# Kernel tuning notes

Hardware: AMD Instinct MI355X
Metric: run time of the kernel (lower is better)

The kernel has to match this reference:

```python
import jax, jax.numpy as jnp
import numpy as np

EMB = 300; H = 150; DEC = 300
VU = 50000; VQ = 30000; VS = 5000
N_COLS = 64; COL_LEN = 6; N_TURNS = 6; IN_LEN = 128; GEN_LEN = 64
MAX_KEEP = 5


def _lstm_cell(x, h, c, Wih, Whh, b):
    z = x @ Wih.T + h @ Whh.T + b
    i, f, g, o = jnp.split(z, 4)
    c = jax.nn.sigmoid(f) * c + jax.nn.sigmoid(i) * jnp.tanh(g)
    h = jax.nn.sigmoid(o) * jnp.tanh(c)
    return h, c


def _run_lstm(xs, Wih, Whh, b):
    hsz = Whh.shape[-1]
    z = jnp.zeros((hsz,), xs.dtype)
    def step(carry, x):
        h, c = _lstm_cell(x, carry[0], carry[1], Wih, Whh, b)
        return (h, c), h
    (h, c), ys = jax.lax.scan(step, (z, z), xs)
    return ys, h, c


def _bilstm(xs, Wih, Whh, b):
    # Wih: [2, 4H, in], Whh: [2, 4H, H], b: [2, 4H]
    yf, hf, cf = _run_lstm(xs, Wih[0], Whh[0], b[0])
    yb, hb, cb = _run_lstm(xs[::-1], Wih[1], Whh[1], b[1])
    return jnp.concatenate([yf, yb[::-1]], -1), jnp.concatenate([hf, hb], -1), jnp.concatenate([cf, cb], -1)


def _attention(q, keys, Wq, Wk, v):
    # Bahdanau: v^T tanh(Wq q + Wk k); context = softmax-weighted sum of keys
    s = jnp.tanh(q @ Wq + keys @ Wk) @ v
    return jax.nn.softmax(s) @ keys


def _forward(utter_emb, query_emb, schema_tok_emb, enc_Wih, enc_Whh, enc_b,
             attn_Wq, attn_Wk, attn_v, dec_Wih0, dec_Whh0, dec_b0,
             dec_Wih1, dec_Whh1, dec_b1, transform_W, sql_W, sql_b, col_W,
             schema_tokens, input_seqs, output_gt):
    attn = lambda k_i, q, keys: _attention(q, keys, attn_Wq[k_i], attn_Wk[k_i], attn_v[k_i])
    # --- schema column encoding: BiLSTM over each column's name tokens ---
    col_tok = schema_tok_emb[schema_tokens]                       # [C, L, EMB]
    _, h, _ = jax.vmap(lambda xs: _bilstm(xs, enc_Wih[0], enc_Whh[0], enc_b[0]))(col_tok)
    schema_embs = h                                               # [C, EMB]
    prev_in, prev_h, prev_c, prev_out = [], [], [], []
    all_dists = []
    bos_emb = query_emb[0]
    for i in range(N_TURNS):
        idx = input_seqs[i]
        # mixed vocab / schema-pointer embedding lookup
        x = jnp.where((idx < VU)[:, None],
                      utter_emb[jnp.clip(idx, 0, VU - 1)],
                      schema_embs[jnp.clip(idx - VU, 0, N_COLS - 1)])
        x, _, _ = _bilstm(x, enc_Wih[1], enc_Whh[1], enc_b[1])    # utter_encoder
        # TextSchemaEncoder (approx): second BiLSTM + schema cross-attention update
        x, fh, fc = _bilstm(x, enc_Wih[2], enc_Whh[2], enc_b[2])
        schema_embs = schema_embs + jax.nn.softmax(schema_embs @ x.T, -1) @ x
        h0, c0 = fh, fc
        if i > 0:
            hist_h = jnp.stack(prev_h); hist_c = jnp.stack(prev_c)
            h0n = h0 + attn(0, h0, hist_h)
            c0 = h0n + attn(0, c0, hist_c)  # replicates original's h-based c init
            h0 = h0n
        prev_in = (prev_in + [x])[:MAX_KEEP]
        prev_h = (prev_h + [fh])[:MAX_KEEP]
        prev_c = (prev_c + [fc])[:MAX_KEEP]
        keys_in = jnp.concatenate(prev_in, 0)
        keys_out = jnp.concatenate(prev_out, 0) if i > 0 else None
        se = schema_embs

        def embed_out(t):
            return jnp.where(t < VQ,
                             query_emb[jnp.clip(t, 0, VQ - 1)],
                             se[jnp.clip(t - VQ, 0, N_COLS - 1)])

        def dec_step(carry, t):
            h1p, c1p, h2p, c2p, dh = carry
            out_emb = embed_out(t)  # teacher forcing
            ctx_s = attn(1, dh, se)
            ctx_i = attn(2, dh, keys_in)
            ctx_o = attn(3, dh, keys_out) if keys_out is not None else jnp.zeros_like(ctx_i)
            ctx = jnp.concatenate([ctx_s, ctx_i, ctx_o])
            xin = jnp.concatenate([out_emb, ctx])                 # [4*EMB]
            h1, c1 = _lstm_cell(xin, h1p, c1p, dec_Wih0, dec_Whh0, dec_b0)
            h2, c2 = _lstm_cell(h1, h2p, c2p, dec_Wih1, dec_Whh1, dec_b1)
            out = jnp.tanh(jnp.concatenate([h2, ctx]) @ transform_W.T)
            score = jnp.concatenate([out @ sql_W.T + sql_b, (out @ col_W.T) @ se.T])
            dist = jax.nn.log_softmax(score)
            am_emb = embed_out(jnp.argmax(dist))
            return (h1, c1, h2, c2, h2), (dist, am_emb)

        init = (h0, c0, h0, c0, h0)
        _, (dists, am_embs) = jax.lax.scan(dec_step, init, output_gt[i, :GEN_LEN - 1])
        prev_out = (prev_out + [jnp.concatenate([bos_emb[None], am_embs], 0)])[:MAX_KEEP]
        all_dists.append(dists)
    return jnp.stack(all_dists, 0)  # [N_TURNS, GEN_LEN-1, VQ+N_COLS]


def setup_inputs() -> dict:
    key = jax.random.key(0)
    ks = jax.random.split(key, 24)
    s = 0.05
    f = lambda k, shape: jax.random.normal(k, shape, jnp.float32) * s
    return {
        "utter_emb": f(ks[0], (VU, EMB)),
        "query_emb": f(ks[1], (VQ, EMB)),
        "schema_tok_emb": f(ks[2], (VS, EMB)),
        "enc_Wih": f(ks[3], (3, 2, 4 * H, EMB)),   # [schema, utter, text-schema] x [fwd, bwd]
        "enc_Whh": f(ks[4], (3, 2, 4 * H, H)),
        "enc_b": f(ks[5], (3, 2, 4 * H)),
        "attn_Wq": f(ks[6], (4, EMB, EMB)),        # [turn, schema, in_tok, out_tok]
        "attn_Wk": f(ks[7], (4, EMB, EMB)),
        "attn_v": f(ks[8], (4, EMB)),
        "dec_Wih0": f(ks[9], (4 * DEC, 4 * EMB)),
        "dec_Whh0": f(ks[10], (4 * DEC, DEC)),
        "dec_b0": f(ks[11], (4 * DEC,)),
        "dec_Wih1": f(ks[12], (4 * DEC, DEC)),
        "dec_Whh1": f(ks[13], (4 * DEC, DEC)),
        "dec_b1": f(ks[14], (4 * DEC,)),
        "transform_W": f(ks[15], (EMB, 4 * EMB)),
        "sql_W": f(ks[16], (VQ, EMB)),
        "sql_b": f(ks[17], (VQ,)),
        "col_W": f(ks[18], (EMB, EMB)),
        "schema_tokens": jax.random.randint(ks[19], (N_COLS, COL_LEN), 0, VS),
        "input_seqs": jax.random.randint(ks[20], (N_TURNS, IN_LEN), 0, VU + N_COLS),
        "output_gt": jax.random.randint(ks[21], (N_TURNS, GEN_LEN), 0, VQ + N_COLS),
    }


def reference(utter_emb, query_emb, schema_tok_emb, enc_Wih, enc_Whh, enc_b,
              attn_Wq, attn_Wk, attn_v, dec_Wih0, dec_Whh0, dec_b0,
              dec_Wih1, dec_Whh1, dec_b1, transform_W, sql_W, sql_b, col_W,
              schema_tokens, input_seqs, output_gt):
    return _forward(utter_emb, query_emb, schema_tok_emb, enc_Wih, enc_Whh, enc_b,
                    attn_Wq, attn_Wk, attn_v, dec_Wih0, dec_Whh0, dec_b0,
                    dec_Wih1, dec_Whh1, dec_b1, transform_W, sql_W, sql_b, col_W,
                    schema_tokens, input_seqs, output_gt)
```

## Files before the change

### kernel.cpp

```cpp
#include <hip/hip_runtime.h>

#define EMB 300
#define VU 50000
#define VQ 30000
#define NCOLS 64
#define COLLEN 6
#define NTURNS 6
#define INLEN 128
#define TSTEPS 63
#define VOUT 30064
#define MAXK 5
#define NWD 60
#define FPAD 32
#define SENTU 0x7FC00001u
#define NGRP 8
#define GQW (TSTEPS*960)
#define GSC (TSTEPS*1024)
#define GH  (TSTEPS*320)

__device__ __forceinline__ float sigf(float x){ return 1.0f/(1.0f+__expf(-x)); }
__device__ __forceinline__ float tanhf_(float x){ return 1.0f - 2.0f/(1.0f+__expf(2.0f*x)); }
__device__ __forceinline__ float wsum(float v){
#pragma unroll
  for (int o=32;o;o>>=1) v += __shfl_xor(v,o);
  return v;
}
__device__ __forceinline__ float wmax(float v){
#pragma unroll
  for (int o=32;o;o>>=1) v = fmaxf(v,__shfl_xor(v,o));
  return v;
}

__device__ __forceinline__ void gstore(float* p, float v){
  __hip_atomic_store((int*)p, __float_as_int(v), __ATOMIC_RELAXED, __HIP_MEMORY_SCOPE_AGENT);
}
__device__ __forceinline__ float gload(const float* p){
  return __int_as_float(__hip_atomic_load((const int*)p, __ATOMIC_RELAXED, __HIP_MEMORY_SCOPE_AGENT));
}
__device__ __forceinline__ void gpub(float* p, float v){
  (void)__hip_atomic_exchange((int*)p, __float_as_int(v), __ATOMIC_RELAXED, __HIP_MEMORY_SCOPE_AGENT);
}

__device__ __forceinline__ void garrive(int* flags, int w, int P){
  asm volatile("s_waitcnt vmcnt(0)" ::: "memory");
  __syncthreads();
  if (threadIdx.x == 0)
    __hip_atomic_store(flags + w*FPAD, P, __ATOMIC_RELAXED, __HIP_MEMORY_SCOPE_AGENT);
}
__device__ __forceinline__ void gwait(const int* flags, int P){
  if (threadIdx.x < 64) {
    int v;
    do {
      v = (threadIdx.x < NWD) ? __hip_atomic_load(flags + threadIdx.x*FPAD, __ATOMIC_RELAXED, __HIP_MEMORY_SCOPE_AGENT) : P;
    } while (__any(v < P));
  }
  __syncthreads();
}

template<int MAXV>
__device__ __forceinline__ void pollfetch(const float* __restrict__ src, float* dstLDS,
                                          int n, int modstride, int tid)
{
  float v[MAXV]; bool val[MAXV]; int idx[MAXV];
#pragma unroll
  for (int k = 0; k < MAXV; ++k) {
    idx[k] = tid + 256*k;
    bool ib = idx[k] < n;
    if (modstride) {
      int m = idx[k];
      while (m >= modstride) m -= modstride;
      ib = ib && (m < 300);
    }
    val[k] = ib;
  }
  for (;;) {
    bool ok = true;
#pragma unroll
    for (int k = 0; k < MAXV; ++k)
      if (val[k]) { v[k] = gload(src + idx[k]); ok = ok && (__float_as_uint(v[k]) != SENTU); }
    if (__all(ok)) break;
    __builtin_amdgcn_s_sleep(1);
  }
#pragma unroll
  for (int k = 0; k < MAXV; ++k) if (val[k]) dstLDS[idx[k]] = v[k];
  __syncthreads();
}

__global__ void k_init(int* flags){
  for (int i = threadIdx.x; i < NWD*FPAD; i += 256) flags[i] = 0;
}

__global__ void k_transposeB(const float* __restrict__ in, float* __restrict__ out,
                             int R, int C, size_t mstride)
{
  __shared__ float tile[32][33];
  const float* inp = in + (size_t)blockIdx.z*mstride;
  float* outp = out + (size_t)blockIdx.z*mstride;
  const int rb = blockIdx.y*32, cb = blockIdx.x*32;
  const int tx = threadIdx.x & 31, ty = threadIdx.x >> 5;
  for (int k = 0; k < 32; k += 8) {
    int r = rb + ty + k, c = cb + tx;
    if (r < R && c < C) tile[ty+k][tx] = inp[(size_t)r*C + c];
  }
  __syncthreads();
  for (int k = 0; k < 32; k += 8) {
    int c = cb + ty + k, r = rb + tx;
    if (c < C && r < R) outp[(size_t)c*R + r] = tile[tx][ty+k];
  }
}

__global__ void k_schema(const float* __restrict__ temb, const int* __restrict__ stok,
                         const float* __restrict__ Wih, const float* __restrict__ Whh,
                         const float* __restrict__ bb, float* __restrict__ SE0)
{
  const int col = blockIdx.x >> 1, dir = blockIdx.x & 1, tid = threadIdx.x;
  __shared__ float hl[150], cl[150], zl[600], xs[304];
  if (tid < 150) { hl[tid]=0.f; cl[tid]=0.f; }
  __syncthreads();
  const float* Wi = Wih + (size_t)dir*600*300;
  const float* Wh = Whh + (size_t)dir*600*150;
  const float* bd = bb + dir*600;
  for (int s = 0; s < COLLEN; ++s) {
    const int pos = dir ? (COLLEN-1-s) : s;
    const int tok = stok[col*COLLEN + pos];
    const float* x = temb + (size_t)tok*300;
    for (int c = tid; c < 300; c += 256) xs[c] = x[c];
    __syncthreads();
    for (int g = tid; g < 600; g += 256) {
      float a = bd[g];
      const float* wi = Wi + (size_t)g*300;
      for (int c = 0; c < 300; ++c) a += xs[c]*wi[c];
      const float* wh = Wh + (size_t)g*150;
      for (int j = 0; j < 150; ++j) a += hl[j]*wh[j];
      zl[g] = a;
    }
    __syncthreads();
    if (tid < 150) {
      float ii=zl[tid], ff=zl[150+tid], gg=zl[300+tid], oo=zl[450+tid];
      float cn = sigf(ff)*cl[tid] + sigf(ii)*tanhf_(gg);
      cl[tid]=cn; hl[tid]=sigf(oo)*tanhf_(cn);
    }
    __syncthreads();
  }
  if (tid < 150) SE0[(size_t)col*300 + dir*150 + tid] = hl[tid];
}

__global__ void k_gemm_xe(const float* __restrict__ src, const float* __restrict__ SEi,
                          const int* __restrict__ iseq, int mode,
                          const float* __restrict__ WihT, const float* __restrict__ bL,
                          float* __restrict__ Xg)
{
  __shared__ float xs[16][304];
  const int tid = threadIdx.x;
  const int p0 = blockIdx.y*16;
  for (int i = tid; i < 16*300; i += 256) {
    int t = i / 300, c = i - t*300;
    const float* xr;
    if (mode) xr = src + (size_t)(p0+t)*300;
    else {
      int tok = iseq[p0+t];
      xr = (tok < VU) ? src + (size_t)tok*300 : SEi + (size_t)(tok - VU)*300;
    }
    xs[t][c] = xr[c];
  }
  __syncthreads();
  const int g = blockIdx.x*256 + tid;
  if (g >= 1200) return;
  const float b = bL[g];
  float acc[16];
#pragma unroll
  for (int t = 0; t < 16; ++t) acc[t] = b;
  for (int c = 0; c < 300; ++c) {
    float wv = WihT[(size_t)c*1200 + g];
#pragma unroll
    for (int t = 0; t < 16; ++t) acc[t] += wv * xs[t][c];
  }
#pragma unroll
  for (int t = 0; t < 16; ++t) Xg[(size_t)(p0+t)*1200 + g] = acc[t];
}

__global__ __launch_bounds__(640) void k_rec(
    const float* __restrict__ Xg, const float* __restrict__ WhhTL,
    float* __restrict__ ys, float* __restrict__ fh, float* __restrict__ fc)
{
  const int dir = blockIdx.x, tid = threadIdx.x;
  __shared__ __align__(16) float hl[2][152];
  const int g = (tid & 3)*150 + (tid >> 2);
  const bool act = (tid < 600);
  float w[150];
  const float* wt = WhhTL + (size_t)dir*150*600;
  if (act) {
#pragma unroll
    for (int j = 0; j < 150; ++j) w[j] = wt[(size_t)j*600 + g];
  }
  if (tid < 152) { hl[0][tid] = 0.f; hl[1][tid] = 0.f; }
  float cr = 0.f;
  __syncthreads();
  int par = 0;
  float xg = act ? Xg[(size_t)(dir ? INLEN-1 : 0)*1200 + dir*600 + g] : 0.f;
  for (int s = 0; s < INLEN; ++s) {
    const int pos = dir ? (INLEN-1-s) : s;
    const int nxt = dir ? (INLEN-2-s) : (s+1);
    float xg_nx = (s+1 < INLEN && act) ? Xg[(size_t)nxt*1200 + dir*600 + g] : 0.f;
    float acc = 0.f;
    if (act) {
      float aa[8];
#pragma unroll
      for (int q = 0; q < 8; ++q) aa[q] = 0.f;
      const float4* h4 = (const float4*)hl[par];
#pragma unroll
      for (int j4 = 0; j4 < 37; ++j4) {
        float4 h = h4[j4];
        aa[j4&7] += w[4*j4]*h.x + w[4*j4+1]*h.y + w[4*j4+2]*h.z + w[4*j4+3]*h.w;
      }
      acc = xg + ((aa[0]+aa[1])+(aa[2]+aa[3])) + ((aa[4]+aa[5])+(aa[6]+aa[7]))
            + w[148]*hl[par][148] + w[149]*hl[par][149];
    }
    float a1 = __shfl_xor(acc, 1);
    float a2 = __shfl_xor(acc, 2);
    float a3 = __shfl_xor(acc, 3);
    if (act && (tid & 3) == 0) {
      int d = tid >> 2;
      float cn = sigf(a1)*cr + sigf(acc)*tanhf_(a2);
      cr = cn;
      float hn = sigf(a3)*tanhf_(cn);
      hl[par^1][d] = hn;
      ys[(size_t)pos*300 + dir*150 + d] = hn;
    }
    __syncthreads();
    par ^= 1;
    xg = xg_nx;
  }
  if (act && (tid & 3) == 0) {
    int d = tid >> 2;
    fh[dir*150 + d] = hl[par][d];
    fc[dir*150 + d] = cr;
  }
}

__global__ void k_schema_upd(const float* __restrict__ SEi, const float* __restrict__ ys2,
                             float* __restrict__ SEo,
                             const float* __restrict__ fh, const float* __restrict__ fc,
                             float* __restrict__ HH, float* __restrict__ CH,
                             float* __restrict__ XH, int turn)
{
  const int row = blockIdx.x, tid = threadIdx.x;
  __shared__ float sl[300], al[128], red[4];
  for (int d = tid; d < 300; d += 256) sl[d] = SEi[(size_t)row*300 + d];
  __syncthreads();
  if (tid < 128) {
    float a = 0;
    const float* yr = ys2 + (size_t)tid*300;
    for (int d = 0; d < 300; ++d) a += sl[d]*yr[d];
    al[tid] = a;
  }
  __syncthreads();
  if (tid < 64) { float m = fmaxf(al[tid], al[tid+64]); m = wmax(m); if (tid==0) red[0]=m; }
  __syncthreads();
  if (tid < 128) al[tid] = __expf(al[tid] - red[0]);
  __syncthreads();
  if (tid < 64) { float s = al[tid] + al[tid+64]; s = wsum(s); if (tid==0) red[1]=s; }
  __syncthreads();
  const float invz = 1.0f/red[1];
  for (int d = tid; d < 300; d += 256) {
    float a = sl[d];
    for (int j = 0; j < 128; ++j) a += (al[j]*invz) * ys2[(size_t)j*300 + d];
    SEo[(size_t)row*300 + d] = a;
  }
  if (turn < MAXK) {
    for (int i = row*600 + tid; i < row*600 + 600; i += 256)
      XH[(size_t)turn*INLEN*300 + i] = ys2[i];
    if (row == 0)
      for (int d = tid; d < 300; d += 256) { HH[turn*300+d] = fh[d]; CH[turn*300+d] = fc[d]; }
  }
}

__device__ __forceinline__ const float* key_ptr(int j, int nin, const float* SE1,
                                                const float* XH, const float* OH, int* fam)
{
  if (j < 64) { *fam = 0; return SE1 + (size_t)j*300; }
  if (j < 64+nin) { *fam = 1; return XH + (size_t)(j-64)*300; }
  *fam = 2; return OH + (size_t)(j-64-nin)*300;
}

__global__ __launch_bounds__(256) void k_tables(
    const float* __restrict__ SE1, const float* __restrict__ XH,
    const float* __restrict__ OH, const float* __restrict__ Wk,
    const float* __restrict__ Wih0T, const float* __restrict__ b0,
    const float* __restrict__ tWT, const float* __restrict__ qemb,
    const int* __restrict__ gt,
    float* __restrict__ KW, float* __restrict__ G2K,
    float* __restrict__ Ew, float* __restrict__ G1KT,
    int nin, int nout)
{
  const int NK = 64 + nin + nout;
  const int NT32 = NK >> 5;
  const int tid = threadIdx.x;
  const int b = blockIdx.x;
  __shared__ float A[32][301];
  const int wv4 = tid >> 6, ln = tid & 63;

  if (b < 2*NT32) {
    const int j0 = (b < NT32 ? b : b - NT32) * 32;
    int fam; const float* base = key_ptr(j0, nin, SE1, XH, OH, &fam);
    for (int jj = wv4*8; jj < wv4*8+8; ++jj)
      for (int c = ln; c < 300; c += 64)
        A[jj][c] = base[(size_t)jj*300 + c];
    __syncthreads();
    if (b < NT32) {
      const float* W = Wk + (size_t)(1+fam)*90000;
      for (int rep = 0; rep < 2; ++rep) {
        int c = tid + rep*256;
        if (c < 300) {
          float acc[32];
#pragma unroll
          for (int j = 0; j < 32; ++j) acc[j] = 0.f;
          for (int d = 0; d < 300; ++d) {
            float wvv = W[(size_t)d*300 + c];
#pragma unroll
            for (int j = 0; j < 32; ++j) acc[j] += A[j][d]*wvv;
          }
#pragma unroll
          for (int j = 0; j < 32; ++j) KW[(size_t)(j0+j)*300 + c] = acc[j];
        }
      }
    } else {
      const int cb = 300 + fam*300;
      for (int rep = 0; rep < 2; ++rep) {
        int r = tid + rep*256;
        if (r < 300) {
          float acc[32];
#pragma unroll
          for (int j = 0; j < 32; ++j) acc[j] = 0.f;
          for (int d = 0; d < 300; ++d) {
            float wvv = tWT[(size_t)(cb+d)*300 + r];
#pragma unroll
            for (int j = 0; j < 32; ++j) acc[j] += A[j][d]*wvv;
          }
#pragma unroll
          for (int j = 0; j < 32; ++j) G2K[(size_t)(j0+j)*300 + r] = acc[j];
        }
      }
    }
  } else if (b < 2*NT32 + 20) {
    const int idx = b - 2*NT32;
    const int gx = idx % 5, ty = idx / 5;
    const int g = gx*256 + tid;
    const int tb = ty*16;
    for (int i = tid; i < 16*300; i += 256) {
      int k = i / 300, c = i - k*300;
      int t = tb + k;
      int tok = (t < 63) ? gt[t] : 0;
      const float* e = (tok < VQ) ? qemb + (size_t)tok*300 : SE1 + (size_t)(tok-VQ)*300;
      A[k][c] = e[c];
    }
    __syncthreads();
    if (g < 1200) {
      float bb = b0[g];
      float acc[16];
#pragma unroll
      for (int k = 0; k < 16; ++k) acc[k] = bb;
      for (int c = 0; c < 300; ++c) {
        float wvv = Wih0T[(size_t)c*1200 + g];
#pragma unroll
        for (int k = 0; k < 16; ++k) acc[k] += wvv * A[k][c];
      }
#pragma unroll
      for (int k = 0; k < 16; ++k)
        if (tb + k < 63) Ew[(size_t)(tb+k)*1200 + g] = acc[k];
    }
  } else {
    const int idx = b - (2*NT32 + 20);
    const int j0 = (idx % NT32)*32, r0 = (idx / NT32)*64;
    int fam; const float* base = key_ptr(j0, nin, SE1, XH, OH, &fam);
    for (int jj = wv4*8; jj < wv4*8+8; ++jj)
      for (int c = ln; c < 300; c += 64)
        A[jj][c] = base[(size_t)jj*300 + c];
    __syncthreads();
    const int r = r0 + (tid & 63);
    const int jg = (tid >> 6)*8;
    const int cb = 300 + fam*300;
    float acc[8] = {0,0,0,0,0,0,0,0};
    if (r < 1200) {
      for (int c = 0; c < 300; ++c) {
        float wvv = Wih0T[(size_t)(cb+c)*1200 + r];
#pragma unroll
        for (int i = 0; i < 8; ++i) acc[i] += A[jg+i][c] * wvv;
      }
#pragma unroll
      for (int i = 0; i < 8; ++i) G1KT[(size_t)r*NK + j0 + jg + i] = acc[i];
    }
  }
}

__global__ __launch_bounds__(256, 1) void k_dec(
    const float* __restrict__ KW, const float* __restrict__ G1KT,
    const float* __restrict__ Ew, const float* __restrict__ WqT,
    const float* __restrict__ av, const float* __restrict__ Wq0,
    const float* __restrict__ Wk0,
    const float* __restrict__ Whh0, const float* __restrict__ Wih1,
    const float* __restrict__ Whh1, const float* __restrict__ b1,
    const float* __restrict__ fh, const float* __restrict__ fc,
    const float* __restrict__ HH, const float* __restrict__ CH,
    float* __restrict__ h0b, float* __restrict__ c0b,
    float* __restrict__ xQW, float* __restrict__ xSC,
    float* __restrict__ xH1, float* __restrict__ xH2,
    float* __restrict__ Alog, float* __restrict__ H2log,
    int nin, int nout, int turn, int* __restrict__ flags)
{
  const int NK = 64 + nin + nout;
  const int w = blockIdx.x, tid = threadIdx.x;
  const int wv = tid >> 6, ln = tid & 63;
  const int grp = w & (NGRP-1);
  __shared__ float g1kl[20][1024];
  __shared__ float kwl[18][320];
  __shared__ float qWlp[3][320];
  __shared__ float vllp[3][320];
  __shared__ float ewl[63][20];
  __shared__ float scl[1024];
  __shared__ float dhl[320], h1l[320];
  __shared__ float pre1[20], pre2[20], zl[20], c1l[5], c2l[5];
  __shared__ float redA[4], alscA[8];
  __shared__ float wr0[4], wr1[4], wr2[4], rm[3], rz[3];
  const float SENTF = __uint_as_float(SENTU);

  for (int i = w*256 + tid; i < NGRP*GQW; i += NWD*256) gstore(xQW + i, SENTF);
  for (int i = w*256 + tid; i < NGRP*GSC; i += NWD*256) gstore(xSC + i, SENTF);
  for (int i = w*256 + tid; i < NGRP*GH;  i += NWD*256) gstore(xH1 + i, SENTF);
  for (int i = w*256 + tid; i < NGRP*GH;  i += NWD*256) gstore(xH2 + i, SENTF);

  for (int i = tid; i < 20*1024; i += 256) {
    int o = i >> 10, j = i & 1023;
    int row = w*5 + (o % 5) + 300*(o / 5);
    g1kl[o][j] = (j < NK) ? G1KT[(size_t)row*NK + j] : 0.f;
  }
  for (int i = tid; i < 18*320; i += 256) {
    int jo = i / 320, c = i - jo*320;
    int j = w*18 + jo;
    kwl[jo][c] = (c < 300 && j < NK) ? KW[(size_t)j*300 + c] : 0.f;
  }
  for (int i = tid; i < 3*320; i += 256) {
    int f = i / 320, c = i - f*320;
    vllp[f][c] = (c < 300) ? av[300 + f*300 + c] : 0.f;
    qWlp[f][c] = 0.f;
  }
  for (int i = tid; i < 63*20; i += 256) {
    int t = i / 20, o = i - t*20;
    int row = w*5 + (o % 5) + 300*(o / 5);
    ewl[t][o] = Ew[(size_t)t*1200 + row];
  }
  if (tid < 20) { dhl[300+tid] = 0.f; h1l[300+tid] = 0.f; }

  float rwh0[5][5], rwh1[5][5], rwi1[5][5], rwq4[4][5], b1r[5];
#pragma unroll
  for (int r = 0; r < 5; ++r) {
    int row = w*5 + r + 300*wv;
    b1r[r] = b1[row];
#pragma unroll
    for (int k = 0; k < 5; ++k) {
      int d = ln + 64*k;
      rwh0[r][k] = (d < 300) ? Whh0[(size_t)row*300 + d] : 0.f;
      rwh1[r][k] = (d < 300) ? Whh1[(size_t)row*300 + d] : 0.f;
      rwi1[r][k] = (d < 300) ? Wih1[(size_t)row*300 + d] : 0.f;
    }
  }
#pragma unroll
  for (int r = 0; r < 4; ++r) {
    int o = r*4 + wv;
    int q = w*15 + ((o < 15) ? o : 0);
    int fam = q / 300, c = q - fam*300;
    const float* bp = WqT + ((size_t)(1+fam)*300 + c)*300;
#pragma unroll
    for (int k = 0; k < 5; ++k) {
      int d = ln + 64*k;
      rwq4[r][k] = (o < 15 && d < 300) ? bp[d] : 0.f;
    }
  }
  const int jlo = (w*18 < NK) ? w*18 : NK-1;
  const int jhi = (w*18+17 < NK) ? w*18+17 : NK-1;
  const int f0 = (jlo < 64) ? 0 : (jlo < 64+nin ? 1 : 2);
  const int f1 = (jhi < 64) ? 0 : (jhi < 64+nin ? 1 : 2);
  __syncthreads();

  if (w == 0) {
    if (turn == 0) {
      for (int d = tid; d < 300; d += 256) { gstore(h0b+d, fh[d]); gstore(c0b+d, fc[d]); }
    } else {
      const int nh = turn;
      for (int d = tid; d < 300; d += 256) dhl[d] = fh[d];
      __syncthreads();
      for (int rep = 0; rep < 2; ++rep) {
        const float* keys = rep ? CH : HH;
        for (int c = tid; c < 300; c += 256) {
          float a = 0;
          for (int d = 0; d < 300; ++d) a += dhl[d]*Wq0[(size_t)d*300 + c];
          h1l[c] = a;
        }
        __syncthreads();
        for (int k = 0; k < nh; ++k) {
          const float* Kr = keys + (size_t)k*300;
          float part = 0;
          for (int c = tid; c < 300; c += 256) {
            float kw = 0;
            for (int d = 0; d < 300; ++d) kw += Kr[d]*Wk0[(size_t)d*300 + c];
            part += av[c]*tanhf_(h1l[c] + kw);
          }
          part = wsum(part);
          if (ln == 0) redA[wv] = part;
          __syncthreads();
          if (tid == 0) alscA[k] = redA[0]+redA[1]+redA[2]+redA[3];
          __syncthreads();
        }
        if (tid == 0) {
          float m = -1e30f;
          for (int k = 0; k < nh; ++k) m = fmaxf(m, alscA[k]);
          float z = 0;
          for (int k = 0; k < nh; ++k) { alscA[k] = __expf(alscA[k]-m); z += alscA[k]; }
          for (int k = 0; k < nh; ++k) alscA[k] /= z;
        }
        __syncthreads();
        if (rep == 0) {
          for (int c = tid; c < 300; c += 256) {
            float a = dhl[c];
            for (int k = 0; k < nh; ++k) a += alscA[k]*keys[(size_t)k*300 + c];
            scl[c] = a; gstore(h0b+c, a);
          }
          __syncthreads();
          for (int d = tid; d < 300; d += 256) dhl[d] = fc[d];
          __syncthreads();
        } else {
          for (int c = tid; c < 300; c += 256) {
            float a = scl[c];
            for (int k = 0; k < nh; ++k) a += alscA[k]*keys[(size_t)k*300 + c];
            gstore(c0b+c, a);
          }
        }
      }
    }
  }
  garrive(flags, w, turn+1);
  gwait(flags, turn+1);

  for (int i = tid; i < 300; i += 256) { float v = gload(h0b+i); dhl[i] = v; h1l[i] = v; }
  if (tid < 5) { float v = gload(c0b + w*5 + tid); c1l[tid] = v; c2l[tid] = v; }
  __syncthreads();

  for (int t = 0; t < TSTEPS; ++t) {
    if (t) pollfetch<2>(xH2 + (size_t)grp*GH + (size_t)(t-1)*320, dhl, 300, 0, tid);
#pragma unroll
    for (int r = 0; r < 4; ++r) {
      float a = 0;
#pragma unroll
      for (int k = 0; k < 5; ++k) a += rwq4[r][k]*dhl[ln + 64*k];
      a = wsum(a);
      int o = r*4 + wv;
      if (ln < NGRP && o < 15) {
        int q = w*15 + o, fam = q/300, c = q - fam*300;
        gpub(xQW + (size_t)ln*GQW + (size_t)t*960 + fam*320 + c, a);
      }
    }
#pragma unroll
    for (int r = 0; r < 5; ++r) {
      float a1 = 0, a2 = 0;
#pragma unroll
      for (int k = 0; k < 5; ++k) {
        float hv = h1l[ln + 64*k], dv = dhl[ln + 64*k];
        a1 += rwh0[r][k]*hv; a2 += rwh1[r][k]*dv;
      }
      a1 = wsum(a1); a2 = wsum(a2);
      if (ln == 0) { pre1[wv*5+r] = a1; pre2[wv*5+r] = a2 + b1r[r]; }
    }

    pollfetch<3>(xQW + (size_t)grp*GQW + (size_t)t*960 + f0*320, &qWlp[f0][0], (f1-f0+1)*320, 320, tid);
#pragma unroll
    for (int r = 0; r < 5; ++r) {
      int jo = wv*5 + r;
      int j = w*18 + jo;
      bool va = (jo < 18) && (j < NK);
      int f = va ? ((j < 64) ? 0 : (j < 64+nin ? 1 : 2)) : 0;
      int jc = (jo < 18) ? jo : 0;
      float a = 0;
#pragma unroll
      for (int k = 0; k < 5; ++k) {
        int c = ln + 64*k;
        a += vllp[f][c] * tanhf_(qWlp[f][c] + kwl[jc][c]);
      }
      a = wsum(a);
      if (ln < NGRP && va) gpub(xSC + (size_t)ln*GSC + (size_t)t*1024 + j, a);
    }

    pollfetch<4>(xSC + (size_t)grp*GSC + (size_t)t*1024, scl, NK, 0, tid);
    {
      float m0=-1e30f, m1=-1e30f, m2=-1e30f;
      for (int j = tid; j < NK; j += 256) {
        float x = scl[j];
        if (j < 64) m0 = fmaxf(m0,x); else if (j < 64+nin) m1 = fmaxf(m1,x); else m2 = fmaxf(m2,x);
      }
      m0 = wmax(m0); m1 = wmax(m1); m2 = wmax(m2);
      if (ln==0){ wr0[wv]=m0; wr1[wv]=m1; wr2[wv]=m2; }
      __syncthreads();
      if (tid==0){
        rm[0]=fmaxf(fmaxf(wr0[0],wr0[1]),fmaxf(wr0[2],wr0[3]));
        rm[1]=fmaxf(fmaxf(wr1[0],wr1[1]),fmaxf(wr1[2],wr1[3]));
        rm[2]=fmaxf(fmaxf(wr2[0],wr2[1]),fmaxf(wr2[2],wr2[3]));
      }
      __syncthreads();
      float s0=0,s1=0,s2=0;
      for (int j = tid; j < NK; j += 256) {
        int f = (j<64)?0:(j<64+nin?1:2);
        float e = __expf(scl[j] - rm[f]);
        scl[j] = e;
        if (f==0) s0+=e; else if (f==1) s1+=e; else s2+=e;
      }
      s0=wsum(s0); s1=wsum(s1); s2=wsum(s2);
      if (ln==0){ wr0[wv]=s0; wr1[wv]=s1; wr2[wv]=s2; }
      __syncthreads();
      if (tid==0){
        rz[0]=wr0[0]+wr0[1]+wr0[2]+wr0[3];
        rz[1]=wr1[0]+wr1[1]+wr1[2]+wr1[3];
        rz[2]=wr2[0]+wr2[1]+wr2[2]+wr2[3];
      }
      __syncthreads();
    }
    const int KC = NK >> 6;
    const int c1e = 1 + (nin >> 6);
    float inv0 = 1.0f/rz[0], inv1 = 1.0f/rz[1];
    float inv2 = (KC > c1e) ? 1.0f/rz[2] : 0.f;
    {
#pragma unroll 1
      for (int r = 0; r < 5; ++r) {
        int o = wv*5 + r;
        float a0 = scl[ln]*g1kl[o][ln];
        float a1 = 0, a2 = 0;
        for (int k = 1; k < c1e; ++k) { int j = ln + 64*k; a1 += scl[j]*g1kl[o][j]; }
        for (int k = c1e; k < KC; ++k) { int j = ln + 64*k; a2 += scl[j]*g1kl[o][j]; }
        float a = a0*inv0 + a1*inv1 + a2*inv2;
        a = wsum(a);
        if (ln == 0) zl[o] = a + ewl[t][o] + pre1[o];
      }
    }
    __syncthreads();
    if (tid < 5) {
      float ii=zl[tid], ff=zl[5+tid], gg=zl[10+tid], oo=zl[15+tid];
      float cn = sigf(ff)*c1l[tid] + sigf(ii)*tanhf_(gg);
      c1l[tid] = cn;
      float h1v = sigf(oo)*tanhf_(cn);
#pragma unroll
      for (int g = 0; g < NGRP; ++g)
        gpub(xH1 + (size_t)g*GH + (size_t)t*320 + w*5 + tid, h1v);
    }
    if (tid < 18) {
      int j = w*18 + tid;
      if (j < NK) {
        int f = (j<64)?0:(j<64+nin?1:2);
        float iv = (f==0)?inv0:((f==1)?inv1:inv2);
        Alog[(size_t)t*1024 + j] = scl[j]*iv;
      }
    }

    pollfetch<2>(xH1 + (size_t)grp*GH + (size_t)t*320, h1l, 300, 0, tid);
#pragma unroll
    for (int r = 0; r < 5; ++r) {
      float a = 0;
#pragma unroll
      for (int k = 0; k < 5; ++k) a += rwi1[r][k]*h1l[ln + 64*k];
      a = wsum(a);
      if (ln == 0) zl[wv*5+r] = a + pre2[wv*5+r];
    }
    __syncthreads();
    if (tid < 5) {
      int d = w*5 + tid;
      float ii=zl[tid], ff=zl[5+tid], gg=zl[10+tid], oo=zl[15+tid];
      float cn = sigf(ff)*c2l[tid] + sigf(ii)*tanhf_(gg);
      c2l[tid] = cn;
      float hn = sigf(oo)*tanhf_(cn);
#pragma unroll
      for (int g = 0; g < NGRP; ++g)
        gpub(xH2 + (size_t)g*GH + (size_t)t*320 + d, hn);
      H2log[(size_t)t*300 + d] = hn;
    }
  }
}

__global__ void k_ctxout2(const float* __restrict__ H2, const float* __restrict__ Al,
                          const float* __restrict__ G2K, const float* __restrict__ tWT,
                          const float* __restrict__ colW,
                          float* __restrict__ o63, float* __restrict__ t63, int NK)
{
  const int t = blockIdx.x, tid = threadIdx.x;
  __shared__ float ol[304], h2l[304], all[1024];
  for (int d = tid; d < 300; d += 256) h2l[d] = H2[(size_t)t*300 + d];
  for (int j = tid; j < NK; j += 256) all[j] = Al[(size_t)t*1024 + j];
  __syncthreads();
  for (int r = tid; r < 300; r += 256) {
    float a = 0;
    for (int d = 0; d < 300; ++d) a += h2l[d]*tWT[(size_t)d*300 + r];
    for (int j = 0; j < NK; ++j) a += all[j]*G2K[(size_t)j*300 + r];
    float v = tanhf_(a);
    ol[r] = v;
    o63[(size_t)t*300 + r] = v;
  }
  __syncthreads();
  for (int e = tid; e < 300; e += 256) {
    float a = 0;
    const float* wc = colW + (size_t)e*300;
    for (int d = 0; d < 300; ++d) a += ol[d]*wc[d];
    t63[(size_t)t*300 + e] = a;
  }
}

__global__ __launch_bounds__(256) void k_score(
    const float* __restrict__ o63, const float* __restrict__ t63,
    const float* __restrict__ sqlW, const float* __restrict__ sqlb,
    const float* __restrict__ SE1, float* __restrict__ Dout)
{
  const int vb = blockIdx.x, tid = threadIdx.x;
  const int v = vb*256 + tid;
  if ((vb+1)*256 <= VQ) {
    __shared__ __align__(16) float olT[300][68];
    for (int i = tid; i < 63*300; i += 256) {
      int k = i / 300, d = i - k*300;
      olT[d][k] = o63[i];
    }
    for (int d = tid; d < 300; d += 256) { olT[d][63] = 0.f; }
    __syncthreads();
    const float* w = sqlW + (size_t)v*300;
    float acc[64];
#pragma unroll
    for (int k = 0; k < 64; ++k) acc[k] = 0.f;
    for (int d = 0; d < 300; ++d) {
      float wv_ = w[d];
      const float4* row = (const float4*)&olT[d][0];
#pragma unroll
      for (int k4 = 0; k4 < 16; ++k4) {
        float4 ov = row[k4];
        acc[k4*4+0] += wv_*ov.x; acc[k4*4+1] += wv_*ov.y;
        acc[k4*4+2] += wv_*ov.z; acc[k4*4+3] += wv_*ov.w;
      }
    }
    const float b = sqlb[v];
    for (int k = 0; k < 63; ++k) Dout[(size_t)k*VOUT + v] = acc[k] + b;
  } else {
    if (v >= VOUT) return;
    const bool isv = (v < VQ);
    const float* w = isv ? sqlW + (size_t)v*300 : SE1 + (size_t)(v - VQ)*300;
    const float* src = isv ? o63 : t63;
    float acc[63];
#pragma unroll
    for (int k = 0; k < 63; ++k) acc[k] = 0.f;
    for (int d = 0; d < 300; ++d) {
      float wv_ = w[d];
      for (int k = 0; k < 63; ++k) acc[k] += wv_ * src[(size_t)k*300 + d];
    }
    const float b = isv ? sqlb[v] : 0.f;
    for (int k = 0; k < 63; ++k) Dout[(size_t)k*VOUT + v] = acc[k] + b;
  }
}

__global__ void k_lsm(float* __restrict__ rows, const float* __restrict__ qemb,
                      const float* __restrict__ SE1, float* __restrict__ OHt)
{
  const int t = blockIdx.x, tid = threadIdx.x, wv = tid>>6, ln = tid&63;
  float* row = rows + (size_t)t*VOUT;
  __shared__ float rv[4], rs[4];
  __shared__ int ri[4];
  float m = -1e30f; int mi = VOUT;
  for (int j = tid; j < VOUT; j += 256) {
    float x = row[j];
    if (x > m) { m = x; mi = j; }
  }
#pragma unroll
  for (int o = 32; o; o >>= 1) {
    float om = __shfl_xor(m, o); int oi = __shfl_xor(mi, o);
    if (om > m || (om == m && oi < mi)) { m = om; mi = oi; }
  }
  if (ln == 0) { rv[wv] = m; ri[wv] = mi; }
  __syncthreads();
  if (tid == 0) {
    for (int k = 1; k < 4; ++k)
      if (rv[k] > rv[0] || (rv[k] == rv[0] && ri[k] < ri[0])) { rv[0]=rv[k]; ri[0]=ri[k]; }
  }
  __syncthreads();
  const float M = rv[0];
  float s = 0;
  for (int j = tid; j < VOUT; j += 256) s += __expf(row[j] - M);
  s = wsum(s);
  if (ln == 0) rs[wv] = s;
  __syncthreads();
  const float L = M + logf(rs[0]+rs[1]+rs[2]+rs[3]);
  for (int j = tid; j < VOUT; j += 256) row[j] -= L;
  if (OHt) {
    int id = ri[0];
    const float* src = (id < VQ) ? qemb + (size_t)id*300 : SE1 + (size_t)(id-VQ)*300;
    for (int d = tid; d < 300; d += 256) {
      OHt[(size_t)(t+1)*300 + d] = src[d];
      if (t == 0) OHt[d] = qemb[d];
    }
  }
}

extern "C" void kernel_launch(void* const* d_in, const int* in_sizes, int n_in,
                              void* d_out, int out_size, void* d_ws, size_t ws_size,
                              hipStream_t stream)
{
  const float* utter = (const float*)d_in[0];
  const float* qemb  = (const float*)d_in[1];
  const float* temb  = (const float*)d_in[2];
  const float* eWih  = (const float*)d_in[3];
  const float* eWhh  = (const float*)d_in[4];
  const float* eb    = (const float*)d_in[5];
  const float* aWq   = (const float*)d_in[6];
  const float* aWk   = (const float*)d_in[7];
  const float* av    = (const float*)d_in[8];
  const float* dWih0 = (const float*)d_in[9];
  const float* dWhh0 = (const float*)d_in[10];
  const float* db0   = (const float*)d_in[11];
  const float* dWih1 = (const float*)d_in[12];
  const float* dWhh1 = (const float*)d_in[13];
  const float* db1   = (const float*)d_in[14];
  const float* tW    = (const float*)d_in[15];
  const float* sqlW  = (const float*)d_in[16];
  const float* sqlb  = (const float*)d_in[17];
  const float* colW  = (const float*)d_in[18];
  const int* stok    = (const int*)d_in[19];
  const int* iseq    = (const int*)d_in[20];
  const int* ogt     = (const int*)d_in[21];
  float* dout = (float*)d_out;

  float* base = (float*)d_ws;
  size_t off = 0;
  auto A = [&](size_t n)->float*{ float* r = base + off; off += (n + 63) & ~(size_t)63; return r; };
  float* SE    = A(7*64*300);
  float* XH    = A(5*128*300);
  float* OH    = A(5*64*300);
  float* HH    = A(5*300);
  float* CH    = A(5*300);
  float* ys1   = A(128*300);
  float* ys2   = A(128*300);
  float* Xg    = A(128*1200);
  float* fh    = A(320);
  float* fc    = A(320);
  float* fhs   = A(320);
  float* fcs   = A(320);
  float* h0b   = A(320);
  float* c0b   = A(320);
  float* xQW   = A(NGRP*GQW);
  float* xSC   = A(NGRP*GSC);
  float* xH1   = A(NGRP*GH);
  float* xH2   = A(NGRP*GH);
  float* KW    = A(1024*300);
  float* G1KT  = A(1200*1024);
  float* G2K   = A(1024*300);
  float* EwB   = A(63*1200);
  float* Alog  = A(63*1024);
  float* H2lg  = A(64*300);
  float* o63   = A(64*300);
  float* t63   = A(64*300);
  A(512);
  float* WqT   = A(4*300*300);
  float* WhhT  = A(6*150*600);
  float* Wih0T = A(1200*1200);
  float* tWT   = A(1200*300);
  float* eWT   = A(2*300*1200);
  int* flags = (int*)A(NWD*FPAD);
  (void)ws_size; (void)in_sizes; (void)n_in; (void)out_size;

  dim3 B256(256);
  k_init<<<1, B256, 0, stream>>>(flags);
  k_transposeB<<<dim3(10,10,4), B256, 0, stream>>>(aWq, WqT, 300, 300, 90000);
  k_transposeB<<<dim3(5,19,6), B256, 0, stream>>>(eWhh, WhhT, 600, 150, 90000);
  k_transposeB<<<dim3(38,38,1), B256, 0, stream>>>(dWih0, Wih0T, 1200, 1200, 0);
  k_transposeB<<<dim3(38,10,1), B256, 0, stream>>>(tW, tWT, 300, 1200, 0);
  k_transposeB<<<dim3(10,38,2), B256, 0, stream>>>(eWih + 360000, eWT, 1200, 300, 360000);
  k_schema<<<128, B256, 0, stream>>>(temb, stok, eWih, eWhh, eb, SE);

  for (int i = 0; i < NTURNS; ++i) {
    const int kin  = (i+1 < MAXK) ? (i+1) : MAXK;
    const int kout = (i < MAXK) ? i : MAXK;
    const int nin = kin*128, nout = kout*64;
    const int NK = 64 + nin + nout;
    const int NT32 = NK/32;
    float* SEi = SE + (size_t)i*19200;
    float* SEo = SE + (size_t)(i+1)*19200;

    k_gemm_xe<<<dim3(5,8), B256, 0, stream>>>(utter, SEi, iseq + i*INLEN, 0,
                                              eWT, eb + 1200, Xg);
    k_rec<<<2, 640, 0, stream>>>(Xg, WhhT + 180000, ys1, fhs, fcs);
    k_gemm_xe<<<dim3(5,8), B256, 0, stream>>>(ys1, SEi, iseq + i*INLEN, 1,
                                              eWT + 360000, eb + 2400, Xg);
    k_rec<<<2, 640, 0, stream>>>(Xg, WhhT + 360000, ys2, fh, fc);
    k_schema_upd<<<64, B256, 0, stream>>>(SEi, ys2, SEo, fh, fc, HH, CH, XH, i);
    k_tables<<<2*NT32 + 20 + NT32*19, B256, 0, stream>>>(
        SEo, XH, OH, aWk, Wih0T, db0, tWT, qemb, ogt + i*64,
        KW, G2K, EwB, G1KT, nin, nout);
    k_dec<<<NWD, B256, 0, stream>>>(KW, G1KT, EwB, WqT, av, aWq, aWk,
                                    dWhh0, dWih1, dWhh1, db1, fh, fc, HH, CH,
                                    h0b, c0b, xQW, xSC, xH1, xH2, Alog, H2lg,
                                    nin, nout, i, flags);
    k_ctxout2<<<63, B256, 0, stream>>>(H2lg, Alog, G2K, tWT, colW, o63, t63, NK);
    k_score<<<dim3(118), B256, 0, stream>>>(o63, t63, sqlW, sqlb, SEo, dout + (size_t)i*63*VOUT);
    k_lsm<<<63, B256, 0, stream>>>(dout + (size_t)i*63*VOUT, qemb, SEo,
                                   (i < MAXK) ? OH + (size_t)i*19200 : nullptr);
  }
}
```

Before: 18.49 ms.

## Fuse per-turn kernel chain into persistent kernels with flag-based grid barriers

Merges the setup transposes, schema encoder and flag init into one k_setup launch. Per turn, the two encoder GEMM and recurrence pairs become one k_enc kernel, schema update plus table building become k_tab, and context output plus scoring become k_ctxsc. Stages inside each fused kernel are separated by software grid barriers on global flags. This cuts launch count and inter-kernel gaps, but relies on all blocks being co-resident, and the fused GEMMs run on only 2 blocks, which may lower parallelism.

```diff
diff --git a/kernel.cpp b/kernel.cpp
--- a/kernel.cpp
+++ b/kernel.cpp
@@ -11,6 +11,8 @@
 #define VOUT 30064
 #define MAXK 5
 #define NWD 60
+#define NWT 720
+#define NWC 240
 #define FPAD 32
 #define SENTU 0x7FC00001u
 #define NGRP 8
@@ -39,6 +41,24 @@
 }
 __device__ __forceinline__ void gpub(float* p, float v){
   (void)__hip_atomic_exchange((int*)p, __float_as_int(v), __ATOMIC_RELAXED, __HIP_MEMORY_SCOPE_AGENT);
+}
+
+__device__ __forceinline__ void fbar(int* flags, int nw, int w, int P)
+{
+  asm volatile("s_waitcnt vmcnt(0)" ::: "memory");
+  __syncthreads();
+  if (threadIdx.x == 0)
+    __hip_atomic_store(flags + w*FPAD, P, __ATOMIC_RELAXED, __HIP_MEMORY_SCOPE_AGENT);
+  if (threadIdx.x < 64) {
+    int ok;
+    do {
+      ok = 1;
+      for (int idx = threadIdx.x; idx < nw; idx += 64)
+        ok &= (__hip_atomic_load(flags + idx*FPAD, __ATOMIC_RELAXED, __HIP_MEMORY_SCOPE_AGENT) >= P);
+      if (!__all(ok)) { ok = 0; __builtin_amdgcn_s_sleep(4); }
+    } while (!ok);
+  }
+  __syncthreads();
 }
 
 __device__ __forceinline__ void garrive(int* flags, int w, int P){
@@ -86,192 +106,197 @@
   __syncthreads();
 }
 
-__global__ void k_init(int* flags){
-  for (int i = threadIdx.x; i < NWD*FPAD; i += 256) flags[i] = 0;
-}
-
-__global__ void k_transposeB(const float* __restrict__ in, float* __restrict__ out,
-                             int R, int C, size_t mstride)
+__device__ __forceinline__ void tr_tile(const float* __restrict__ in, float* __restrict__ out,
+                                        int R, int C, int bx, int by,
+                                        float (*tile)[33], int tid)
+{
+  const int rb = by*32, cb = bx*32;
+  const int tx = tid & 31, ty = (tid >> 5) & 7;
+  for (int k = 0; k < 32; k += 8) {
+    int r = rb + ty + k, c = cb + tx;
+    if (r < R && c < C) tile[ty+k][tx] = in[(size_t)r*C + c];
+  }
+  __syncthreads();
+  for (int k = 0; k < 32; k += 8) {
+    int c = cb + ty + k, r = rb + tx;
+    if (c < C && r < R) out[(size_t)c*R + r] = tile[tx][ty+k];
+  }
+  __syncthreads();
+}
+
+__global__ __launch_bounds__(256) void k_setup(
+    const float* __restrict__ aWq, float* __restrict__ WqT,
+    const float* __restrict__ eWhh, float* __restrict__ WhhT,
+    const float* __restrict__ dWih0, float* __restrict__ Wih0T,
+    const float* __restrict__ tW, float* __restrict__ tWT,
+    const float* __restrict__ eWih, float* __restrict__ eWT,
+    const float* __restrict__ temb, const int* __restrict__ stok,
+    const float* __restrict__ eb, float* __restrict__ SE0,
+    int* __restrict__ eflags, int* __restrict__ tflags,
+    int* __restrict__ cflags, int* __restrict__ dflags)
 {
   __shared__ float tile[32][33];
-  const float* inp = in + (size_t)blockIdx.z*mstride;
-  float* outp = out + (size_t)blockIdx.z*mstride;
-  const int rb = blockIdx.y*32, cb = blockIdx.x*32;
-  const int tx = threadIdx.x & 31, ty = threadIdx.x >> 5;
-  for (int k = 0; k < 32; k += 8) {
-    int r = rb + ty + k, c = cb + tx;
-    if (r < R && c < C) tile[ty+k][tx] = inp[(size_t)r*C + c];
-  }
-  __syncthreads();
-  for (int k = 0; k < 32; k += 8) {
-    int c = cb + ty + k, r = rb + tx;
-    if (c < C && r < R) outp[(size_t)c*R + r] = tile[tx][ty+k];
-  }
-}
-
-__global__ void k_schema(const float* __restrict__ temb, const int* __restrict__ stok,
-                         const float* __restrict__ Wih, const float* __restrict__ Whh,
-                         const float* __restrict__ bb, float* __restrict__ SE0)
-{
-  const int col = blockIdx.x >> 1, dir = blockIdx.x & 1, tid = threadIdx.x;
-  __shared__ float hl[150], cl[150], zl[600], xs[304];
-  if (tid < 150) { hl[tid]=0.f; cl[tid]=0.f; }
-  __syncthreads();
-  const float* Wi = Wih + (size_t)dir*600*300;
-  const float* Wh = Whh + (size_t)dir*600*150;
-  const float* bd = bb + dir*600;
-  for (int s = 0; s < COLLEN; ++s) {
-    const int pos = dir ? (COLLEN-1-s) : s;
-    const int tok = stok[col*COLLEN + pos];
-    const float* x = temb + (size_t)tok*300;
-    for (int c = tid; c < 300; c += 256) xs[c] = x[c];
-    __syncthreads();
-    for (int g = tid; g < 600; g += 256) {
-      float a = bd[g];
-      const float* wi = Wi + (size_t)g*300;
-      for (int c = 0; c < 300; ++c) a += xs[c]*wi[c];
-      const float* wh = Wh + (size_t)g*150;
-      for (int j = 0; j < 150; ++j) a += hl[j]*wh[j];
-      zl[g] = a;
-    }
-    __syncthreads();
-    if (tid < 150) {
-      float ii=zl[tid], ff=zl[150+tid], gg=zl[300+tid], oo=zl[450+tid];
-      float cn = sigf(ff)*cl[tid] + sigf(ii)*tanhf_(gg);
-      cl[tid]=cn; hl[tid]=sigf(oo)*tanhf_(cn);
-    }
-    __syncthreads();
-  }
-  if (tid < 150) SE0[(size_t)col*300 + dir*150 + tid] = hl[tid];
-}
-
-__global__ void k_gemm_xe(const float* __restrict__ src, const float* __restrict__ SEi,
-                          const int* __restrict__ iseq, int mode,
-                          const float* __restrict__ WihT, const float* __restrict__ bL,
-                          float* __restrict__ Xg)
-{
-  __shared__ float xs[16][304];
+  __shared__ float hl[152], cl[152], zl[600], xsr[304];
   const int tid = threadIdx.x;
-  const int p0 = blockIdx.y*16;
-  for (int i = tid; i < 16*300; i += 256) {
-    int t = i / 300, c = i - t*300;
-    const float* xr;
-    if (mode) xr = src + (size_t)(p0+t)*300;
-    else {
-      int tok = iseq[p0+t];
-      xr = (tok < VU) ? src + (size_t)tok*300 : SEi + (size_t)(tok - VU)*300;
-    }
-    xs[t][c] = xr[c];
-  }
-  __syncthreads();
-  const int g = blockIdx.x*256 + tid;
-  if (g >= 1200) return;
-  const float b = bL[g];
-  float acc[16];
-#pragma unroll
-  for (int t = 0; t < 16; ++t) acc[t] = b;
-  for (int c = 0; c < 300; ++c) {
-    float wv = WihT[(size_t)c*1200 + g];
-#pragma unroll
-    for (int t = 0; t < 16; ++t) acc[t] += wv * xs[t][c];
-  }
-#pragma unroll
-  for (int t = 0; t < 16; ++t) Xg[(size_t)(p0+t)*1200 + g] = acc[t];
-}
-
-__global__ __launch_bounds__(640) void k_rec(
-    const float* __restrict__ Xg, const float* __restrict__ WhhTL,
-    float* __restrict__ ys, float* __restrict__ fh, float* __restrict__ fc)
+  const int NCH = 3554 + 128 + 1;
+  for (int ch = blockIdx.x; ch < NCH; ch += 240) {
+    __syncthreads();
+    if (ch < 400) {
+      int z = ch/100, r = ch - z*100;
+      tr_tile(aWq + (size_t)z*90000, WqT + (size_t)z*90000, 300, 300, r%10, r/10, tile, tid);
+    } else if (ch < 970) {
+      int c2 = ch - 400; int z = c2/95, r = c2 - z*95;
+      tr_tile(eWhh + (size_t)z*90000, WhhT + (size_t)z*90000, 600, 150, r%5, r/5, tile, tid);
+    } else if (ch < 2414) {
+      int c2 = ch - 970;
+      tr_tile(dWih0, Wih0T, 1200, 1200, c2%38, c2/38, tile, tid);
+    } else if (ch < 2794) {
+      int c2 = ch - 2414;
+      tr_tile(tW, tWT, 300, 1200, c2%38, c2/38, tile, tid);
+    } else if (ch < 3554) {
+      int c2 = ch - 2794; int z = c2/380, r = c2 - z*380;
+      tr_tile(eWih + 360000 + (size_t)z*360000, eWT + (size_t)z*360000, 1200, 300, r%10, r/10, tile, tid);
+    } else if (ch < 3682) {
+      const int unit = ch - 3554;
+      const int col = unit >> 1, dir = unit & 1;
+      if (tid < 152) { hl[tid]=0.f; cl[tid]=0.f; }
+      __syncthreads();
+      const float* Wi = eWih + (size_t)dir*180000;
+      const float* Wh = eWhh + (size_t)dir*90000;
+      const float* bd = eb + dir*600;
+      for (int s = 0; s < COLLEN; ++s) {
+        const int pos = dir ? (COLLEN-1-s) : s;
+        const int tok = stok[col*COLLEN + pos];
+        const float* x = temb + (size_t)tok*300;
+        for (int c = tid; c < 300; c += 256) xsr[c] = x[c];
+        __syncthreads();
+        for (int g = tid; g < 600; g += 256) {
+          float a = bd[g];
+          const float* wi = Wi + (size_t)g*300;
+          for (int c = 0; c < 300; ++c) a += xsr[c]*wi[c];
+          const float* wh = Wh + (size_t)g*150;
+          for (int j = 0; j < 150; ++j) a += hl[j]*wh[j];
+          zl[g] = a;
+        }
+        __syncthreads();
+        if (tid < 150) {
+          float ii=zl[tid], ff=zl[150+tid], gg=zl[300+tid], oo=zl[450+tid];
+          float cn = sigf(ff)*cl[tid] + sigf(ii)*tanhf_(gg);
+          cl[tid]=cn; hl[tid]=sigf(oo)*tanhf_(cn);
+        }
+        __syncthreads();
+      }
+      if (tid < 150) SE0[(size_t)col*300 + dir*150 + tid] = hl[tid];
+      __syncthreads();
+    } else {
+      for (int i = tid; i < 2*FPAD;   i += 256) eflags[i] = 0;
+      for (int i = tid; i < NWT*FPAD; i += 256) tflags[i] = 0;
+      for (int i = tid; i < NWC*FPAD; i += 256) cflags[i] = 0;
+      for (int i = tid; i < NWD*FPAD; i += 256) dflags[i] = 0;
+    }
+  }
+}
+
+__global__ __launch_bounds__(640) void k_enc(
+    const float* __restrict__ utter, const float* __restrict__ SEi,
+    const int* __restrict__ iseq,
+    const float* __restrict__ eWT, const float* __restrict__ eb,
+    const float* __restrict__ WhhT,
+    float* __restrict__ Xg, float* __restrict__ ys1, float* __restrict__ ys2,
+    float* __restrict__ fh, float* __restrict__ fc,
+    int turn, int* __restrict__ eflags)
 {
   const int dir = blockIdx.x, tid = threadIdx.x;
+  __shared__ float xs[16][304];
   __shared__ __align__(16) float hl[2][152];
-  const int g = (tid & 3)*150 + (tid >> 2);
-  const bool act = (tid < 600);
-  float w[150];
-  const float* wt = WhhTL + (size_t)dir*150*600;
-  if (act) {
-#pragma unroll
-    for (int j = 0; j < 150; ++j) w[j] = wt[(size_t)j*600 + g];
-  }
-  if (tid < 152) { hl[0][tid] = 0.f; hl[1][tid] = 0.f; }
-  float cr = 0.f;
-  __syncthreads();
-  int par = 0;
-  float xg = act ? Xg[(size_t)(dir ? INLEN-1 : 0)*1200 + dir*600 + g] : 0.f;
-  for (int s = 0; s < INLEN; ++s) {
-    const int pos = dir ? (INLEN-1-s) : s;
-    const int nxt = dir ? (INLEN-2-s) : (s+1);
-    float xg_nx = (s+1 < INLEN && act) ? Xg[(size_t)nxt*1200 + dir*600 + g] : 0.f;
-    float acc = 0.f;
-    if (act) {
-      float aa[8];
-#pragma unroll
-      for (int q = 0; q < 8; ++q) aa[q] = 0.f;
-      const float4* h4 = (const float4*)hl[par];
-#pragma unroll
-      for (int j4 = 0; j4 < 37; ++j4) {
-        float4 h = h4[j4];
-        aa[j4&7] += w[4*j4]*h.x + w[4*j4+1]*h.y + w[4*j4+2]*h.z + w[4*j4+3]*h.w;
-      }
-      acc = xg + ((aa[0]+aa[1])+(aa[2]+aa[3])) + ((aa[4]+aa[5])+(aa[6]+aa[7]))
-            + w[148]*hl[par][148] + w[149]*hl[par][149];
-    }
-    float a1 = __shfl_xor(acc, 1);
-    float a2 = __shfl_xor(acc, 2);
-    float a3 = __shfl_xor(acc, 3);
-    if (act && (tid & 3) == 0) {
-      int d = tid >> 2;
-      float cn = sigf(a1)*cr + sigf(acc)*tanhf_(a2);
-      cr = cn;
-      float hn = sigf(a3)*tanhf_(cn);
-      hl[par^1][d] = hn;
-      ys[(size_t)pos*300 + dir*150 + d] = hn;
-    }
-    __syncthreads();
-    par ^= 1;
-    xg = xg_nx;
-  }
-  if (act && (tid & 3) == 0) {
-    int d = tid >> 2;
-    fh[dir*150 + d] = hl[par][d];
-    fc[dir*150 + d] = cr;
-  }
-}
-
-__global__ void k_schema_upd(const float* __restrict__ SEi, const float* __restrict__ ys2,
-                             float* __restrict__ SEo,
-                             const float* __restrict__ fh, const float* __restrict__ fc,
-                             float* __restrict__ HH, float* __restrict__ CH,
-                             float* __restrict__ XH, int turn)
-{
-  const int row = blockIdx.x, tid = threadIdx.x;
-  __shared__ float sl[300], al[128], red[4];
-  for (int d = tid; d < 300; d += 256) sl[d] = SEi[(size_t)row*300 + d];
-  __syncthreads();
-  if (tid < 128) {
-    float a = 0;
-    const float* yr = ys2 + (size_t)tid*300;
-    for (int d = 0; d < 300; ++d) a += sl[d]*yr[d];
-    al[tid] = a;
-  }
-  __syncthreads();
-  if (tid < 64) { float m = fmaxf(al[tid], al[tid+64]); m = wmax(m); if (tid==0) red[0]=m; }
-  __syncthreads();
-  if (tid < 128) al[tid] = __expf(al[tid] - red[0]);
-  __syncthreads();
-  if (tid < 64) { float s = al[tid] + al[tid+64]; s = wsum(s); if (tid==0) red[1]=s; }
-  __syncthreads();
-  const float invz = 1.0f/red[1];
-  for (int d = tid; d < 300; d += 256) {
-    float a = sl[d];
-    for (int j = 0; j < 128; ++j) a += (al[j]*invz) * ys2[(size_t)j*300 + d];
-    SEo[(size_t)row*300 + d] = a;
-  }
-  if (turn < MAXK) {
-    for (int i = row*600 + tid; i < row*600 + 600; i += 256)
-      XH[(size_t)turn*INLEN*300 + i] = ys2[i];
-    if (row == 0)
-      for (int d = tid; d < 300; d += 256) { HH[turn*300+d] = fh[d]; CH[turn*300+d] = fc[d]; }
+
+  for (int layer = 0; layer < 2; ++layer) {
+    const float* WT = eWT + (size_t)layer*360000;
+    const float* bL = eb + 1200 + layer*1200;
+    for (int pt = 0; pt < 8; ++pt) {
+      for (int i = tid; i < 4800; i += 640) {
+        int t = i/300, c = i - t*300;
+        int p = pt*16 + t;
+        float v;
+        if (layer == 0) {
+          int tok = iseq[p];
+          v = (tok < VU) ? utter[(size_t)tok*300 + c] : SEi[(size_t)(tok-VU)*300 + c];
+        } else v = gload(ys1 + (size_t)p*300 + c);
+        xs[t][c] = v;
+      }
+      __syncthreads();
+      if (tid < 600) {
+        int g = dir*600 + tid;
+        float b = bL[g];
+        float acc[16];
+#pragma unroll
+        for (int t = 0; t < 16; ++t) acc[t] = b;
+        for (int c = 0; c < 300; ++c) {
+          float wv = WT[(size_t)c*1200 + g];
+#pragma unroll
+          for (int t = 0; t < 16; ++t) acc[t] += wv * xs[t][c];
+        }
+#pragma unroll
+        for (int t = 0; t < 16; ++t) Xg[(size_t)(pt*16+t)*1200 + g] = acc[t];
+      }
+      __syncthreads();
+    }
+    {
+      const float* wtb = WhhT + (size_t)(2+2*layer)*90000 + (size_t)dir*90000;
+      const int g = (tid & 3)*150 + (tid >> 2);
+      const bool act = (tid < 600);
+      float w_[150];
+      if (act) {
+#pragma unroll
+        for (int j = 0; j < 150; ++j) w_[j] = wtb[(size_t)j*600 + g];
+      }
+      if (tid < 152) { hl[0][tid] = 0.f; hl[1][tid] = 0.f; }
+      float cr = 0.f;
+      __syncthreads();
+      int par = 0;
+      float xg = act ? Xg[(size_t)(dir ? INLEN-1 : 0)*1200 + dir*600 + g] : 0.f;
+      float* ys_ = layer ? ys2 : ys1;
+      for (int s = 0; s < INLEN; ++s) {
+        const int pos = dir ? (INLEN-1-s) : s;
+        const int nxt = dir ? (INLEN-2-s) : (s+1);
+        float xg_nx = (s+1 < INLEN && act) ? Xg[(size_t)nxt*1200 + dir*600 + g] : 0.f;
+        float acc = 0.f;
+        if (act) {
+          float aa[8];
+#pragma unroll
+          for (int q = 0; q < 8; ++q) aa[q] = 0.f;
+          const float4* h4 = (const float4*)hl[par];
+#pragma unroll
+          for (int j4 = 0; j4 < 37; ++j4) {
+            float4 h = h4[j4];
+            aa[j4&7] += w_[4*j4]*h.x + w_[4*j4+1]*h.y + w_[4*j4+2]*h.z + w_[4*j4+3]*h.w;
+          }
+          acc = xg + ((aa[0]+aa[1])+(aa[2]+aa[3])) + ((aa[4]+aa[5])+(aa[6]+aa[7]))
+                + w_[148]*hl[par][148] + w_[149]*hl[par][149];
+        }
+        float a1 = __shfl_xor(acc, 1);
+        float a2 = __shfl_xor(acc, 2);
+        float a3 = __shfl_xor(acc, 3);
+        if (act && (tid & 3) == 0) {
+          int d = tid >> 2;
+          float cn = sigf(a1)*cr + sigf(acc)*tanhf_(a2);
+          cr = cn;
+          float hn = sigf(a3)*tanhf_(cn);
+          hl[par^1][d] = hn;
+          if (layer) ys_[(size_t)pos*300 + dir*150 + d] = hn;
+          else gstore(ys_ + (size_t)pos*300 + dir*150 + d, hn);
+        }
+        __syncthreads();
+        par ^= 1;
+        xg = xg_nx;
+      }
+      if (layer == 1 && act && (tid & 3) == 0) {
+        int d = tid >> 2;
+        fh[dir*150 + d] = hl[par][d];
+        fc[dir*150 + d] = cr;
+      }
+    }
+    if (layer == 0) fbar(eflags, 2, dir, turn+1);
   }
 }
 
@@ -283,113 +308,154 @@
   *fam = 2; return OH + (size_t)(j-64-nin)*300;
 }
 
-__global__ __launch_bounds__(256) void k_tables(
-    const float* __restrict__ SE1, const float* __restrict__ XH,
-    const float* __restrict__ OH, const float* __restrict__ Wk,
-    const float* __restrict__ Wih0T, const float* __restrict__ b0,
-    const float* __restrict__ tWT, const float* __restrict__ qemb,
-    const int* __restrict__ gt,
+__global__ __launch_bounds__(256) void k_tab(
+    const float* __restrict__ SEi, const float* __restrict__ ys2,
+    const float* __restrict__ fh, const float* __restrict__ fc,
+    float* __restrict__ SEo, float* __restrict__ HH, float* __restrict__ CH,
+    float* __restrict__ XH, const float* __restrict__ OH,
+    const float* __restrict__ aWk, const float* __restrict__ Wih0T,
+    const float* __restrict__ b0, const float* __restrict__ tWT,
+    const float* __restrict__ qemb, const int* __restrict__ gt,
     float* __restrict__ KW, float* __restrict__ G2K,
     float* __restrict__ Ew, float* __restrict__ G1KT,
-    int nin, int nout)
+    int nin, int nout, int turn, int* __restrict__ tflags)
 {
-  const int NK = 64 + nin + nout;
-  const int NT32 = NK >> 5;
-  const int tid = threadIdx.x;
-  const int b = blockIdx.x;
+  const int w = blockIdx.x, tid = threadIdx.x;
+  const int ln = tid & 63, wv4 = tid >> 6;
+  const int NK = 64 + nin + nout, NT32 = NK >> 5;
   __shared__ float A[32][301];
-  const int wv4 = tid >> 6, ln = tid & 63;
-
-  if (b < 2*NT32) {
-    const int j0 = (b < NT32 ? b : b - NT32) * 32;
-    int fam; const float* base = key_ptr(j0, nin, SE1, XH, OH, &fam);
-    for (int jj = wv4*8; jj < wv4*8+8; ++jj)
-      for (int c = ln; c < 300; c += 64)
-        A[jj][c] = base[(size_t)jj*300 + c];
-    __syncthreads();
-    if (b < NT32) {
-      const float* W = Wk + (size_t)(1+fam)*90000;
-      for (int rep = 0; rep < 2; ++rep) {
-        int c = tid + rep*256;
-        if (c < 300) {
-          float acc[32];
-#pragma unroll
-          for (int j = 0; j < 32; ++j) acc[j] = 0.f;
-          for (int d = 0; d < 300; ++d) {
-            float wvv = W[(size_t)d*300 + c];
-#pragma unroll
-            for (int j = 0; j < 32; ++j) acc[j] += A[j][d]*wvv;
+  __shared__ float sl[304], al[128], red2[4];
+
+  if (w < 64) {
+    const int row = w;
+    for (int d = tid; d < 300; d += 256) sl[d] = SEi[(size_t)row*300 + d];
+    __syncthreads();
+    if (tid < 128) {
+      float a = 0;
+      const float* yr = ys2 + (size_t)tid*300;
+      for (int d = 0; d < 300; ++d) a += sl[d]*yr[d];
+      al[tid] = a;
+    }
+    __syncthreads();
+    if (tid < 64) { float m = fmaxf(al[tid], al[tid+64]); m = wmax(m); if (tid==0) red2[0]=m; }
+    __syncthreads();
+    if (tid < 128) al[tid] = __expf(al[tid] - red2[0]);
+    __syncthreads();
+    if (tid < 64) { float s = al[tid] + al[tid+64]; s = wsum(s); if (tid==0) red2[1]=s; }
+    __syncthreads();
+    const float invz = 1.0f/red2[1];
+    for (int d = tid; d < 300; d += 256) {
+      float a = sl[d];
+      for (int j = 0; j < 128; ++j) a += (al[j]*invz) * ys2[(size_t)j*300 + d];
+      gstore(SEo + (size_t)row*300 + d, a);
+    }
+    if (turn < MAXK) {
+      for (int i = row*600 + tid; i < row*600 + 600; i += 256)
+        gstore(XH + (size_t)turn*INLEN*300 + i, ys2[i]);
+      if (row == 0)
+        for (int d = tid; d < 300; d += 256) {
+          gstore(HH + turn*300 + d, fh[d]);
+          gstore(CH + turn*300 + d, fc[d]);
+        }
+    }
+  }
+  fbar(tflags, NWT, w, turn+1);
+
+  const int nch = 2*NT32 + 20 + NT32*19;
+  for (int b = w; b < nch; b += NWT) {
+    __syncthreads();
+    if (b < 2*NT32) {
+      const int j0 = (b < NT32 ? b : b - NT32) * 32;
+      int fam; const float* base = key_ptr(j0, nin, SEo, XH, OH, &fam);
+      for (int jj = wv4*8; jj < wv4*8+8; ++jj)
+        for (int c = ln; c < 300; c += 64)
+          A[jj][c] = gload(base + (size_t)jj*300 + c);
+      __syncthreads();
+      if (b < NT32) {
+        const float* W = aWk + (size_t)(1+fam)*90000;
+        for (int rep = 0; rep < 2; ++rep) {
+          int c = tid + rep*256;
+          if (c < 300) {
+            float acc[32];
+#pragma unroll
+            for (int j = 0; j < 32; ++j) acc[j] = 0.f;
+            for (int d = 0; d < 300; ++d) {
+              float wvv = W[(size_t)d*300 + c];
+#pragma unroll
+              for (int j = 0; j < 32; ++j) acc[j] += A[j][d]*wvv;
+            }
+#pragma unroll
+            for (int j = 0; j < 32; ++j) KW[(size_t)(j0+j)*300 + c] = acc[j];
           }
-#pragma unroll
-          for (int j = 0; j < 32; ++j) KW[(size_t)(j0+j)*300 + c] = acc[j];
-        }
+        }
+      } else {
+        const int cb = 300 + fam*300;
+        for (int rep = 0; rep < 2; ++rep) {
+          int r = tid + rep*256;
+          if (r < 300) {
+            float acc[32];
+#pragma unroll
+            for (int j = 0; j < 32; ++j) acc[j] = 0.f;
+            for (int d = 0; d < 300; ++d) {
+              float wvv = tWT[(size_t)(cb+d)*300 + r];
+#pragma unroll
+              for (int j = 0; j < 32; ++j) acc[j] += A[j][d]*wvv;
+            }
+#pragma unroll
+            for (int j = 0; j < 32; ++j) G2K[(size_t)(j0+j)*300 + r] = acc[j];
+          }
+        }
+      }
+    } else if (b < 2*NT32 + 20) {
+      const int idx = b - 2*NT32;
+      const int gx = idx % 5, ty = idx / 5;
+      const int g = gx*256 + tid;
+      const int tb = ty*16;
+      for (int i = tid; i < 16*300; i += 256) {
+        int k = i / 300, c = i - k*300;
+        int t = tb + k;
+        int tok = (t < 63) ? gt[t] : 0;
+        A[k][c] = (tok < VQ) ? qemb[(size_t)tok*300 + c]
+                             : gload(SEo + (size_t)(tok-VQ)*300 + c);
+      }
+      __syncthreads();
+      if (g < 1200) {
+        float bb = b0[g];
+        float acc[16];
+#pragma unroll
+        for (int k = 0; k < 16; ++k) acc[k] = bb;
+        for (int c = 0; c < 300; ++c) {
+          float wvv = Wih0T[(size_t)c*1200 + g];
+#pragma unroll
+          for (int k = 0; k < 16; ++k) acc[k] += wvv * A[k][c];
+        }
+#pragma unroll
+        for (int k = 0; k < 16; ++k)
+          if (tb + k < 63) Ew[(size_t)(tb+k)*1200 + g] = acc[k];
       }
     } else {
+      const int idx = b - (2*NT32 + 20);
+      const int j0 = (idx % NT32)*32, r0 = (idx / NT32)*64;
+      int fam; const float* base = key_ptr(j0, nin, SEo, XH, OH, &fam);
+      for (int jj = wv4*8; jj < wv4*8+8; ++jj)
+        for (int c = ln; c < 300; c += 64)
+          A[jj][c] = gload(base + (size_t)jj*300 + c);
+      __syncthreads();
+      const int r = r0 + (tid & 63);
+      const int jg = (tid >> 6)*8;
       const int cb = 300 + fam*300;
-      for (int rep = 0; rep < 2; ++rep) {
-        int r = tid + rep*256;
-        if (r < 300) {
-          float acc[32];
-#pragma unroll
-          for (int j = 0; j < 32; ++j) acc[j] = 0.f;
-          for (int d = 0; d < 300; ++d) {
-            float wvv = tWT[(size_t)(cb+d)*300 + r];
-#pragma unroll
-            for (int j = 0; j < 32; ++j) acc[j] += A[j][d]*wvv;
-          }
-#pragma unroll
-          for (int j = 0; j < 32; ++j) G2K[(size_t)(j0+j)*300 + r] = acc[j];
-        }
-      }
-    }
-  } else if (b < 2*NT32 + 20) {
-    const int idx = b - 2*NT32;
-    const int gx = idx % 5, ty = idx / 5;
-    const int g = gx*256 + tid;
-    const int tb = ty*16;
-    for (int i = tid; i < 16*300; i += 256) {
-      int k = i / 300, c = i - k*300;
-      int t = tb + k;
-      int tok = (t < 63) ? gt[t] : 0;
-      const float* e = (tok < VQ) ? qemb + (size_t)tok*300 : SE1 + (size_t)(tok-VQ)*300;
-      A[k][c] = e[c];
-    }
-    __syncthreads();
-    if (g < 1200) {
-      float bb = b0[g];
-      float acc[16];
-#pragma unroll
-      for (int k = 0; k < 16; ++k) acc[k] = bb;
-      for (int c = 0; c < 300; ++c) {
-        float wvv = Wih0T[(size_t)c*1200 + g];
-#pragma unroll
-        for (int k = 0; k < 16; ++k) acc[k] += wvv * A[k][c];
-      }
-#pragma unroll
-      for (int k = 0; k < 16; ++k)
-        if (tb + k < 63) Ew[(size_t)(tb+k)*1200 + g] = acc[k];
-    }
-  } else {
-    const int idx = b - (2*NT32 + 20);
-    const int j0 = (idx % NT32)*32, r0 = (idx / NT32)*64;
-    int fam; const float* base = key_ptr(j0, nin, SE1, XH, OH, &fam);
-    for (int jj = wv4*8; jj < wv4*8+8; ++jj)
-      for (int c = ln; c < 300; c += 64)
-        A[jj][c] = base[(size_t)jj*300 + c];
-    __syncthreads();
-    const int r = r0 + (tid & 63);
-    const int jg = (tid >> 6)*8;
-    const int cb = 300 + fam*300;
-    float acc[8] = {0,0,0,0,0,0,0,0};
-    if (r < 1200) {
-      for (int c = 0; c < 300; ++c) {
-        float wvv = Wih0T[(size_t)(cb+c)*1200 + r];
-#pragma unroll
-        for (int i = 0; i < 8; ++i) acc[i] += A[jg+i][c] * wvv;
-      }
-#pragma unroll
-      for (int i = 0; i < 8; ++i) G1KT[(size_t)r*NK + j0 + jg + i] = acc[i];
-    }
+      float acc[8] = {0,0,0,0,0,0,0,0};
+      if (r < 1200) {
+        for (int c = 0; c < 300; ++c) {
+          float wvv = Wih0T[(size_t)(cb+c)*1200 + r];
+#pragma unroll
+          for (int i = 0; i < 8; ++i) acc[i] += A[jg+i][c] * wvv;
+        }
+#pragma unroll
+        for (int i = 0; i < 8; ++i) G1KT[(size_t)r*NK + j0 + jg + i] = acc[i];
+      }
+    }
+    __syncthreads();
   }
 }
 
@@ -682,78 +748,121 @@
   }
 }
 
-__global__ void k_ctxout2(const float* __restrict__ H2, const float* __restrict__ Al,
-                          const float* __restrict__ G2K, const float* __restrict__ tWT,
-                          const float* __restrict__ colW,
-                          float* __restrict__ o63, float* __restrict__ t63, int NK)
+__global__ __launch_bounds__(256) void k_ctxsc(
+    const float* __restrict__ H2, const float* __restrict__ Al,
+    const float* __restrict__ G2K, const float* __restrict__ tWT,
+    const float* __restrict__ colW,
+    float* __restrict__ o63, float* __restrict__ t63,
+    const float* __restrict__ sqlW, const float* __restrict__ sqlb,
+    const float* __restrict__ SEo, float* __restrict__ Dout,
+    int NK, int turn, int* __restrict__ cflags)
 {
-  const int t = blockIdx.x, tid = threadIdx.x;
+  const int w = blockIdx.x, tid = threadIdx.x;
+  __shared__ __align__(16) float olT[300][68];
   __shared__ float ol[304], h2l[304], all[1024];
-  for (int d = tid; d < 300; d += 256) h2l[d] = H2[(size_t)t*300 + d];
-  for (int j = tid; j < NK; j += 256) all[j] = Al[(size_t)t*1024 + j];
-  __syncthreads();
-  for (int r = tid; r < 300; r += 256) {
-    float a = 0;
-    for (int d = 0; d < 300; ++d) a += h2l[d]*tWT[(size_t)d*300 + r];
-    for (int j = 0; j < NK; ++j) a += all[j]*G2K[(size_t)j*300 + r];
-    float v = tanhf_(a);
-    ol[r] = v;
-    o63[(size_t)t*300 + r] = v;
-  }
-  __syncthreads();
-  for (int e = tid; e < 300; e += 256) {
-    float a = 0;
-    const float* wc = colW + (size_t)e*300;
-    for (int d = 0; d < 300; ++d) a += ol[d]*wc[d];
-    t63[(size_t)t*300 + e] = a;
-  }
-}
-
-__global__ __launch_bounds__(256) void k_score(
-    const float* __restrict__ o63, const float* __restrict__ t63,
-    const float* __restrict__ sqlW, const float* __restrict__ sqlb,
-    const float* __restrict__ SE1, float* __restrict__ Dout)
-{
-  const int vb = blockIdx.x, tid = threadIdx.x;
-  const int v = vb*256 + tid;
-  if ((vb+1)*256 <= VQ) {
-    __shared__ __align__(16) float olT[300][68];
+
+  if (w < 63) {
+    const int t = w;
+    for (int d = tid; d < 300; d += 256) h2l[d] = H2[(size_t)t*300 + d];
+    for (int j = tid; j < NK; j += 256) all[j] = Al[(size_t)t*1024 + j];
+    __syncthreads();
+    for (int r = tid; r < 300; r += 256) {
+      float a = 0;
+      for (int d = 0; d < 300; ++d) a += h2l[d]*tWT[(size_t)d*300 + r];
+      for (int j = 0; j < NK; ++j) a += all[j]*G2K[(size_t)j*300 + r];
+      float v = tanhf_(a);
+      ol[r] = v;
+      gstore(o63 + (size_t)t*300 + r, v);
+    }
+    __syncthreads();
+    for (int e = tid; e < 300; e += 256) {
+      float a = 0;
+      const float* wc = colW + (size_t)e*300;
+      for (int d = 0; d < 300; ++d) a += ol[d]*wc[d];
+      gstore(t63 + (size_t)t*300 + e, a);
+    }
+  }
+  fbar(cflags, NWC, w, turn+1);
+
+  if (w < 118) {
+    const int vb = w;
+    const int v = vb*256 + tid;
     for (int i = tid; i < 63*300; i += 256) {
       int k = i / 300, d = i - k*300;
-      olT[d][k] = o63[i];
-    }
-    for (int d = tid; d < 300; d += 256) { olT[d][63] = 0.f; }
-    __syncthreads();
-    const float* w = sqlW + (size_t)v*300;
-    float acc[64];
-#pragma unroll
-    for (int k = 0; k < 64; ++k) acc[k] = 0.f;
-    for (int d = 0; d < 300; ++d) {
-      float wv_ = w[d];
-      const float4* row = (const float4*)&olT[d][0];
-#pragma unroll
-      for (int k4 = 0; k4 < 16; ++k4) {
-        float4 ov = row[k4];
-        acc[k4*4+0] += wv_*ov.x; acc[k4*4+1] += wv_*ov.y;
-        acc[k4*4+2] += wv_*ov.z; acc[k4*4+3] += wv_*ov.w;
-      }
-    }
-    const float b = sqlb[v];
-    for (int k = 0; k < 63; ++k) Dout[(size_t)k*VOUT + v] = acc[k] + b;
-  } else {
-    if (v >= VOUT) return;
-    const bool isv = (v < VQ);
-    const float* w = isv ? sqlW + (size_t)v*300 : SE1 + (size_t)(v - VQ)*300;
-    const float* src = isv ? o63 : t63;
-    float acc[63];
-#pragma unroll
-    for (int k = 0; k < 63; ++k) acc[k] = 0.f;
-    for (int d = 0; d < 300; ++d) {
-      float wv_ = w[d];
-      for (int k = 0; k < 63; ++k) acc[k] += wv_ * src[(size_t)k*300 + d];
-    }
-    const float b = isv ? sqlb[v] : 0.f;
-    for (int k = 0; k < 63; ++k) Dout[(size_t)k*VOUT + v] = acc[k] + b;
+      olT[d][k] = gload(o63 + i);
+    }
+    for (int d = tid; d < 300; d += 256) olT[d][63] = 0.f;
+    __syncthreads();
+    if ((vb+1)*256 <= VQ) {
+      const float4* w4 = (const float4*)(sqlW + (size_t)v*300);
+      float acc[64];
+#pragma unroll
+      for (int k = 0; k < 64; ++k) acc[k] = 0.f;
+      for (int d4 = 0; d4 < 75; ++d4) {
+        float4 wq = w4[d4];
+        float wa[4] = {wq.x, wq.y, wq.z, wq.w};
+#pragma unroll
+        for (int s = 0; s < 4; ++s) {
+          float ws = wa[s];
+          const float4* row = (const float4*)&olT[d4*4+s][0];
+#pragma unroll
+          for (int k4 = 0; k4 < 16; ++k4) {
+            float4 ov = row[k4];
+            acc[4*k4+0] += ws*ov.x; acc[4*k4+1] += ws*ov.y;
+            acc[4*k4+2] += ws*ov.z; acc[4*k4+3] += ws*ov.w;
+          }
+        }
+      }
+      const float b = sqlb[v];
+      for (int k = 0; k < 63; ++k) Dout[(size_t)k*VOUT + v] = acc[k] + b;
+    } else {
+      if (v < VQ) {
+        const float4* w4 = (const float4*)(sqlW + (size_t)v*300);
+        float acc[64];
+#pragma unroll
+        for (int k = 0; k < 64; ++k) acc[k] = 0.f;
+        for (int d4 = 0; d4 < 75; ++d4) {
+          float4 wq = w4[d4];
+          float wa[4] = {wq.x, wq.y, wq.z, wq.w};
+#pragma unroll
+          for (int s = 0; s < 4; ++s) {
+            float ws = wa[s];
+            const float4* row = (const float4*)&olT[d4*4+s][0];
+#pragma unroll
+            for (int k4 = 0; k4 < 16; ++k4) {
+              float4 ov = row[k4];
+              acc[4*k4+0] += ws*ov.x; acc[4*k4+1] += ws*ov.y;
+              acc[4*k4+2] += ws*ov.z; acc[4*k4+3] += ws*ov.w;
+            }
+          }
+        }
+        const float b = sqlb[v];
+        for (int k = 0; k < 63; ++k) Dout[(size_t)k*VOUT + v] = acc[k] + b;
+      }
+      __syncthreads();
+      for (int i = tid; i < 63*300; i += 256) {
+        int k = i / 300, d = i - k*300;
+        olT[d][k] = gload(t63 + i);
+      }
+      __syncthreads();
+      if (v >= VQ && v < VOUT) {
+        const float* wrow = SEo + (size_t)(v - VQ)*300;
+        float acc[64];
+#pragma unroll
+        for (int k = 0; k < 64; ++k) acc[k] = 0.f;
+        for (int d = 0; d < 300; ++d) {
+          float ws = wrow[d];
+          const float4* row = (const float4*)&olT[d][0];
+#pragma unroll
+          for (int k4 = 0; k4 < 16; ++k4) {
+            float4 ov = row[k4];
+            acc[4*k4+0] += ws*ov.x; acc[4*k4+1] += ws*ov.y;
+            acc[4*k4+2] += ws*ov.z; acc[4*k4+3] += ws*ov.w;
+          }
+        }
+        for (int k = 0; k < 63; ++k) Dout[(size_t)k*VOUT + v] = acc[k];
+      }
+    }
   }
 }
 
@@ -840,8 +949,6 @@
   float* Xg    = A(128*1200);
   float* fh    = A(320);
   float* fc    = A(320);
-  float* fhs   = A(320);
-  float* fcs   = A(320);
   float* h0b   = A(320);
   float* c0b   = A(320);
   float* xQW   = A(NGRP*GQW);
@@ -862,44 +969,37 @@
   float* Wih0T = A(1200*1200);
   float* tWT   = A(1200*300);
   float* eWT   = A(2*300*1200);
-  int* flags = (int*)A(NWD*FPAD);
+  int* eflags = (int*)A(2*FPAD);
+  int* tflags = (int*)A(NWT*FPAD);
+  int* cflags = (int*)A(NWC*FPAD);
+  int* dflags = (int*)A(NWD*FPAD);
   (void)ws_size; (void)in_sizes; (void)n_in; (void)out_size;
 
-  dim3 B256(256);
-  k_init<<<1, B256, 0, stream>>>(flags);
-  k_transposeB<<<dim3(10,10,4), B256, 0, stream>>>(aWq, WqT, 300, 300, 90000);
-  k_transposeB<<<dim3(5,19,6), B256, 0, stream>>>(eWhh, WhhT, 600, 150, 90000);
-  k_transposeB<<<dim3(38,38,1), B256, 0, stream>>>(dWih0, Wih0T, 1200, 1200, 0);
-  k_transposeB<<<dim3(38,10,1), B256, 0, stream>>>(tW, tWT, 300, 1200, 0);
-  k_transposeB<<<dim3(10,38,2), B256, 0, stream>>>(eWih + 360000, eWT, 1200, 300, 360000);
-  k_schema<<<128, B256, 0, stream>>>(temb, stok, eWih, eWhh, eb, SE);
+  k_setup<<<240, 256, 0, stream>>>(aWq, WqT, eWhh, WhhT, dWih0, Wih0T, tW, tWT,
+                                   eWih, eWT, temb, stok, eb, SE,
+                                   eflags, tflags, cflags, dflags);
 
   for (int i = 0; i < NTURNS; ++i) {
     const int kin  = (i+1 < MAXK) ? (i+1) : MAXK;
     const int kout = (i < MAXK) ? i : MAXK;
     const int nin = kin*128, nout = kout*64;
     const int NK = 64 + nin + nout;
-    const int NT32 = NK/32;
     float* SEi = SE + (size_t)i*19200;
     float* SEo = SE + (size_t)(i+1)*19200;
 
-    k_gemm_xe<<<dim3(5,8), B256, 0, stream>>>(utter, SEi, iseq + i*INLEN, 0,
-                                              eWT, eb + 1200, Xg);
-    k_rec<<<2, 640, 0, stream>>>(Xg, WhhT + 180000, ys1, fhs, fcs);
-    k_gemm_xe<<<dim3(5,8), B256, 0, stream>>>(ys1, SEi, iseq + i*INLEN, 1,
-                                              eWT + 360000, eb + 2400, Xg);
-    k_rec<<<2, 640, 0, stream>>>(Xg, WhhT + 360000, ys2, fh, fc);
-    k_schema_upd<<<64, B256, 0, stream>>>(SEi, ys2, SEo, fh, fc, HH, CH, XH, i);
-    k_tables<<<2*NT32 + 20 + NT32*19, B256, 0, stream>>>(
-        SEo, XH, OH, aWk, Wih0T, db0, tWT, qemb, ogt + i*64,
-        KW, G2K, EwB, G1KT, nin, nout);
-    k_dec<<<NWD, B256, 0, stream>>>(KW, G1KT, EwB, WqT, av, aWq, aWk,
-                                    dWhh0, dWih1, dWhh1, db1, fh, fc, HH, CH,
-                                    h0b, c0b, xQW, xSC, xH1, xH2, Alog, H2lg,
-                                    nin, nout, i, flags);
-    k_ctxout2<<<63, B256, 0, stream>>>(H2lg, Alog, G2K, tWT, colW, o63, t63, NK);
-    k_score<<<dim3(118), B256, 0, stream>>>(o63, t63, sqlW, sqlb, SEo, dout + (size_t)i*63*VOUT);
-    k_lsm<<<63, B256, 0, stream>>>(dout + (size_t)i*63*VOUT, qemb, SEo,
-                                   (i < MAXK) ? OH + (size_t)i*19200 : nullptr);
-  }
-}
+    k_enc<<<2, 640, 0, stream>>>(utter, SEi, iseq + i*INLEN, eWT, eb, WhhT,
+                                 Xg, ys1, ys2, fh, fc, i, eflags);
+    k_tab<<<NWT, 256, 0, stream>>>(SEi, ys2, fh, fc, SEo, HH, CH, XH, OH,
+                                   aWk, Wih0T, db0, tWT, qemb, ogt + i*64,
+                                   KW, G2K, EwB, G1KT, nin, nout, i, tflags);
+    k_dec<<<NWD, 256, 0, stream>>>(KW, G1KT, EwB, WqT, av, aWq, aWk,
+                                   dWhh0, dWih1, dWhh1, db1, fh, fc, HH, CH,
+                                   h0b, c0b, xQW, xSC, xH1, xH2, Alog, H2lg,
+                                   nin, nout, i, dflags);
+    k_ctxsc<<<NWC, 256, 0, stream>>>(H2lg, Alog, G2K, tWT, colW, o63, t63,
+                                     sqlW, sqlb, SEo, dout + (size_t)i*63*VOUT,
+                                     NK, i, cflags);
+    k_lsm<<<63, 256, 0, stream>>>(dout + (size_t)i*63*VOUT, qemb, SEo,
+                                  (i < MAXK) ? OH + (size_t)i*19200 : nullptr);
+  }
+}
```

New measurement: 28.86 ms. +56.1%, slower.
